# Performance work log

Measured on AMD Instinct MI355X. Metric: run time of the kernel, lower is better.

## Reference

```python
import jax, jax.numpy as jnp
import numpy as np


def setup_inputs() -> dict:
    key = jax.random.key(0)
    k1, k2 = jax.random.split(key)
    N, B, E, H = 2048, 8, 256, 512
    x = jax.random.normal(k1, (N, B, E), dtype=jnp.float32)
    h = jax.random.normal(k2, (N, B, H), dtype=jnp.float32)
    return {"x": x, "h": h}


def reference(x, h):
    # x: (N, B, E), h: (N, B, H)
    H = h.shape[-1]
    xt = jnp.transpose(x, (1, 0, 2))            # (B, N, E)
    norm = jnp.linalg.norm(xt, axis=2, keepdims=True)  # (B, N, 1)
    xn = xt / norm
    # cosine-similarity scores, softmax over keys (last dim)
    scores = jax.nn.softmax(jnp.einsum('bie,bje->bij', xn, xn), axis=2)  # (B, N, N)
    ht = jnp.transpose(h, (1, 0, 2))            # (B, N, H)
    # The original expands scores/h over an H-fold dim, bmm's, and sums;
    # that equals H * (scores @ h). Keep the H factor for faithfulness
    # (it cancels in the global-norm division below).
    g = H * jnp.einsum('bij,bjh->bih', scores, ht)  # (B, N, H)
    g = jnp.transpose(g, (1, 0, 2))             # (N, B, H)
    return g / jnp.linalg.norm(g)
```

## Files before the change

kernel.cpp:

```cpp
#include <hip/hip_runtime.h>
#include <hip/hip_bf16.h>

#define N_TOK 2048
#define B_SZ  8
#define E_DIM 256
#define H_DIM 512
#define ITERS (N_TOK / 32)

typedef __attribute__((ext_vector_type(8))) short bf16x8;
typedef __attribute__((ext_vector_type(4))) float f32x4;

__device__ __forceinline__ unsigned short f2bf(float f) {
    union { float f; unsigned u; } v; v.f = f;
    unsigned r = v.u + 0x7FFF + ((v.u >> 16) & 1);
    return (unsigned short)(r >> 16);
}
__device__ __forceinline__ float bf2f(unsigned short b) {
    union { unsigned u; float f; } v; v.u = ((unsigned)b) << 16;
    return v.f;
}

__global__ void prep_kernel(const float* __restrict__ x,
                            const float* __restrict__ hptr,
                            unsigned short* __restrict__ Xn,
                            unsigned short* __restrict__ Vp) {
    int bid = blockIdx.x;
    int t = threadIdx.x;
    if (bid < N_TOK * B_SZ) {
        int r = bid;
        int i = r >> 3, b = r & 7;
        float v = x[(size_t)r * E_DIM + t];
        float s = v * v;
        #pragma unroll
        for (int o = 32; o > 0; o >>= 1) s += __shfl_xor(s, o);
        __shared__ float red[4];
        int lane = t & 63, w = t >> 6;
        if (lane == 0) red[w] = s;
        __syncthreads();
        float tot = red[0] + red[1] + red[2] + red[3];
        float rn = 1.0f / sqrtf(tot);
        int u = t >> 3, lo = t & 7;
        Xn[((size_t)b * N_TOK + i) * E_DIM + (size_t)((u ^ (i & 7)) * 8 + lo)] =
            f2bf(v * rn);
    } else {
        int lin = bid - N_TOK * B_SZ;
        int jb = lin & 63, hb = (lin >> 6) & 15, b = lin >> 10;
        __shared__ float tile[32][33];
        int j0 = jb * 32, h0 = hb * 32;
        int tx = t & 31, ty = t >> 5;
        #pragma unroll
        for (int it = 0; it < 4; it++) {
            int j = j0 + ty + it * 8;
            tile[ty + it * 8][tx] = hptr[((size_t)j * B_SZ + b) * H_DIM + h0 + tx];
        }
        __syncthreads();
        size_t base = ((size_t)b * (N_TOK / 32) + jb) * (H_DIM * 32);
        #pragma unroll
        for (int it = 0; it < 4; it++) {
            int hc = h0 + ty + it * 8;
            int jg = tx >> 3, swz = (hc >> 1) & 3;
            Vp[base + (size_t)(hc * 4 + (jg ^ swz)) * 8 + (tx & 7)] =
                f2bf(tile[tx][ty + it * 8]);
        }
    }
}

#define PT_STRIDE 40

__launch_bounds__(256, 2)
__global__ void flash_kernel(const unsigned short* __restrict__ Xn,
                             const unsigned short* __restrict__ Vp,
                             float* __restrict__ out,
                             float* __restrict__ sumsq) {
    __shared__ __attribute__((aligned(16))) unsigned short Kbuf[2][32 * 256];
    __shared__ __attribute__((aligned(16))) unsigned short Pt[4][16 * PT_STRIDE];

    int b  = blockIdx.x;
    int q0 = blockIdx.y * 32;
    int t = threadIdx.x;
    int w = t >> 6, lane = t & 63;
    int quad = lane >> 4, nm = lane & 15;
    int rg = w >> 1, hh = w & 1;

    const unsigned short* Kbase = Xn + (size_t)b * N_TOK * E_DIM;
    const unsigned short* Qrow =
        Xn + ((size_t)b * N_TOK + q0 + rg * 16 + nm) * E_DIM;
    const unsigned short* Vtile0 = Vp + (size_t)b * (N_TOK / 32) * (H_DIM * 32);

    bf16x8 qf[8];
    #pragma unroll
    for (int ec = 0; ec < 8; ec++)
        qf[ec] = *(const bf16x8*)(Qrow + (size_t)(((ec * 4 + quad) ^ (nm & 7)) * 8));

    f32x4 O[16];
    #pragma unroll
    for (int i = 0; i < 16; i++) O[i] = (f32x4){0.f, 0.f, 0.f, 0.f};
    float l_lane[4];
    #pragma unroll
    for (int r = 0; r < 4; r++) l_lane[r] = 0.0f;

    auto stage = [&](int tile, int buf) {
        const unsigned short* src0 = Kbase + (size_t)tile * 32 * E_DIM;
        #pragma unroll
        for (int k = 0; k < 4; k++) {
            int chunk = w * 4 + k;
            __builtin_amdgcn_global_load_lds(
                (const __attribute__((address_space(1))) unsigned int*)
                    (src0 + (size_t)chunk * 512 + lane * 8),
                (__attribute__((address_space(3))) unsigned int*)
                    (&Kbuf[buf][chunk * 512]),
                16, 0, 0);
        }
    };

    stage(0, 0);
    int vswz = (quad ^ ((nm >> 1) & 3)) * 8;

    for (int it = 0; it < ITERS; ++it) {
        __syncthreads();
        int cur = it & 1;

        const unsigned short* Vt = Vtile0 + (size_t)it * (H_DIM * 32);
        bf16x8 vf[16];
        #pragma unroll
        for (int tt = 0; tt < 16; tt++) {
            int hc = hh * 256 + tt * 16 + nm;
            vf[tt] = *(const bf16x8*)(Vt + (size_t)(hc * 4) * 8 + vswz);
        }

        if (it + 1 < ITERS) stage(it + 1, cur ^ 1);
        const unsigned short* KB = &Kbuf[cur][0];

        f32x4 s0 = (f32x4){0.f,0.f,0.f,0.f}, s1 = (f32x4){0.f,0.f,0.f,0.f};
        #pragma unroll
        for (int ec = 0; ec < 8; ec++) {
            int u = ((ec * 4 + quad) ^ (nm & 7)) * 8;
            bf16x8 kf0 = *(const bf16x8*)(KB + nm * 256 + u);
            bf16x8 kf1 = *(const bf16x8*)(KB + (16 + nm) * 256 + u);
            s0 = __builtin_amdgcn_mfma_f32_16x16x32_bf16(qf[ec], kf0, s0, 0, 0, 0);
            s1 = __builtin_amdgcn_mfma_f32_16x16x32_bf16(qf[ec], kf1, s1, 0, 0, 0);
        }

        #pragma unroll
        for (int r = 0; r < 4; r++) {
            unsigned short pb0 = f2bf(__expf(s0[r] - 1.0f));
            unsigned short pb1 = f2bf(__expf(s1[r] - 1.0f));
            l_lane[r] += bf2f(pb0) + bf2f(pb1);
            Pt[w][(quad * 4 + r) * PT_STRIDE + nm]      = pb0;
            Pt[w][(quad * 4 + r) * PT_STRIDE + 16 + nm] = pb1;
        }

        asm volatile("s_waitcnt lgkmcnt(0)" ::: "memory");
        __builtin_amdgcn_wave_barrier();
        bf16x8 pf = *(const bf16x8*)(&Pt[w][nm * PT_STRIDE + quad * 8]);

        #pragma unroll
        for (int tt = 0; tt < 16; tt++)
            O[tt] = __builtin_amdgcn_mfma_f32_16x16x32_bf16(pf, vf[tt], O[tt], 0, 0, 0);
    }

    float linv[4];
    #pragma unroll
    for (int r = 0; r < 4; r++) {
        float lv = l_lane[r];
        #pragma unroll
        for (int o = 1; o < 16; o <<= 1) lv += __shfl_xor(lv, o);
        linv[r] = 1.0f / lv;
    }

    float ss = 0.0f;
    #pragma unroll
    for (int tt = 0; tt < 16; tt++) {
        #pragma unroll
        for (int r = 0; r < 4; r++) {
            float val = O[tt][r] * linv[r];
            int row = q0 + rg * 16 + quad * 4 + r;
            int col = hh * 256 + tt * 16 + nm;
            out[((size_t)row * B_SZ + b) * H_DIM + col] = val;
            ss += val * val;
        }
    }
    #pragma unroll
    for (int o = 1; o < 64; o <<= 1) ss += __shfl_xor(ss, o);
    if (lane == 0) atomicAdd(sumsq, ss);
}

__global__ void scale_kernel(float* __restrict__ out,
                             const float* __restrict__ sumsq) {
    size_t idx = ((size_t)blockIdx.x * blockDim.x + threadIdx.x) * 4;
    float rs = 1.0f / sqrtf(*sumsq);
    float4 v = *(float4*)(out + idx);
    v.x *= rs; v.y *= rs; v.z *= rs; v.w *= rs;
    *(float4*)(out + idx) = v;
}

extern "C" void kernel_launch(void* const* d_in, const int* in_sizes, int n_in,
                              void* d_out, int out_size, void* d_ws, size_t ws_size,
                              hipStream_t stream) {
    const float* x = (const float*)d_in[0];
    const float* h = (const float*)d_in[1];
    float* out = (float*)d_out;

    unsigned short* Xn = (unsigned short*)d_ws;
    unsigned short* Vp = Xn + (size_t)B_SZ * N_TOK * E_DIM;
    float* sumsq = (float*)(Vp + (size_t)B_SZ * N_TOK * H_DIM);

    hipMemsetAsync(sumsq, 0, sizeof(float), stream);
    prep_kernel<<<N_TOK * B_SZ + (N_TOK / 32) * (H_DIM / 32) * B_SZ,
                  256, 0, stream>>>(x, h, Xn, Vp);
    flash_kernel<<<dim3(B_SZ, N_TOK / 32), 256, 0, stream>>>(Xn, Vp, out, sumsq);
    scale_kernel<<<out_size / (4 * 256), 256, 0, stream>>>(out, sumsq);
}
```

Measured before the change: 227.1 us.

## Split key range across two wave groups in flash kernel and vectorize prep

The flash kernel now launches 512 threads per block, and two groups of four waves each process half of the key tiles. Their partial O and l accumulators are combined through LDS at the end, before normalization and the sum-of-squares atomic. This roughly doubles the waves in flight per query block, which helps hide latency for a grid of only 512 blocks. It costs more LDS per block, an extra reduction step, and tighter register limits from the 512,4 launch bounds. The prep kernel also switches to one wave per row with float4 loads and packed 4-element bf16 stores for both the X normalization and the V transpose.

```diff
diff --git a/kernel.cpp b/kernel.cpp
--- a/kernel.cpp
+++ b/kernel.cpp
@@ -1,14 +1,14 @@
 #include <hip/hip_runtime.h>
-#include <hip/hip_bf16.h>
 
 #define N_TOK 2048
 #define B_SZ  8
 #define E_DIM 256
 #define H_DIM 512
-#define ITERS (N_TOK / 32)
+#define TPG   (N_TOK / 64)
 
 typedef __attribute__((ext_vector_type(8))) short bf16x8;
 typedef __attribute__((ext_vector_type(4))) float f32x4;
+typedef __attribute__((ext_vector_type(4))) unsigned short u16x4;
 
 __device__ __forceinline__ unsigned short f2bf(float f) {
     union { float f; unsigned u; } v; v.f = f;
@@ -26,24 +26,23 @@
                             unsigned short* __restrict__ Vp) {
     int bid = blockIdx.x;
     int t = threadIdx.x;
-    if (bid < N_TOK * B_SZ) {
-        int r = bid;
-        int i = r >> 3, b = r & 7;
-        float v = x[(size_t)r * E_DIM + t];
-        float s = v * v;
+    if (bid < (N_TOK * B_SZ) / 4) {
+        int w = t >> 6, lane = t & 63;
+        int r = bid * 4 + w;
+        int n = r >> 3, b = r & 7;
+        float4 v = *(const float4*)(x + (size_t)r * E_DIM + lane * 4);
+        float s = v.x * v.x + v.y * v.y + v.z * v.z + v.w * v.w;
         #pragma unroll
         for (int o = 32; o > 0; o >>= 1) s += __shfl_xor(s, o);
-        __shared__ float red[4];
-        int lane = t & 63, w = t >> 6;
-        if (lane == 0) red[w] = s;
-        __syncthreads();
-        float tot = red[0] + red[1] + red[2] + red[3];
-        float rn = 1.0f / sqrtf(tot);
-        int u = t >> 3, lo = t & 7;
-        Xn[((size_t)b * N_TOK + i) * E_DIM + (size_t)((u ^ (i & 7)) * 8 + lo)] =
-            f2bf(v * rn);
+        float rn = 1.0f / sqrtf(s);
+        u16x4 pk;
+        pk[0] = f2bf(v.x * rn); pk[1] = f2bf(v.y * rn);
+        pk[2] = f2bf(v.z * rn); pk[3] = f2bf(v.w * rn);
+        int u = lane >> 1, half = lane & 1;
+        *(u16x4*)(Xn + ((size_t)b * N_TOK + n) * E_DIM
+                     + (size_t)((u ^ (n & 7)) * 8 + half * 4)) = pk;
     } else {
-        int lin = bid - N_TOK * B_SZ;
+        int lin = bid - (N_TOK * B_SZ) / 4;
         int jb = lin & 63, hb = (lin >> 6) & 15, b = lin >> 10;
         __shared__ float tile[32][33];
         int j0 = jb * 32, h0 = hb * 32;
@@ -55,32 +54,33 @@
         }
         __syncthreads();
         size_t base = ((size_t)b * (N_TOK / 32) + jb) * (H_DIM * 32);
-        #pragma unroll
-        for (int it = 0; it < 4; it++) {
-            int hc = h0 + ty + it * 8;
-            int jg = tx >> 3, swz = (hc >> 1) & 3;
-            Vp[base + (size_t)(hc * 4 + (jg ^ swz)) * 8 + (tx & 7)] =
-                f2bf(tile[tx][ty + it * 8]);
-        }
+        int hcl = t >> 3, jg = (t >> 1) & 3, half = t & 1;
+        int hc = h0 + hcl;
+        u16x4 pk;
+        #pragma unroll
+        for (int k = 0; k < 4; k++)
+            pk[k] = f2bf(tile[jg * 8 + half * 4 + k][hcl]);
+        *(u16x4*)(Vp + base + (size_t)(hc * 4 + (jg ^ ((hcl >> 1) & 3))) * 8
+                     + half * 4) = pk;
     }
 }
 
 #define PT_STRIDE 40
 
-__launch_bounds__(256, 2)
+__launch_bounds__(512, 4)
 __global__ void flash_kernel(const unsigned short* __restrict__ Xn,
                              const unsigned short* __restrict__ Vp,
                              float* __restrict__ out,
                              float* __restrict__ sumsq) {
-    __shared__ __attribute__((aligned(16))) unsigned short Kbuf[2][32 * 256];
-    __shared__ __attribute__((aligned(16))) unsigned short Pt[4][16 * PT_STRIDE];
+    __shared__ __attribute__((aligned(16))) unsigned short Kbuf[2][2][32 * 256];
+    __shared__ __attribute__((aligned(16))) unsigned short Pt[8][16 * PT_STRIDE];
 
     int b  = blockIdx.x;
     int q0 = blockIdx.y * 32;
     int t = threadIdx.x;
     int w = t >> 6, lane = t & 63;
     int quad = lane >> 4, nm = lane & 15;
-    int rg = w >> 1, hh = w & 1;
+    int ks = w >> 2, rg = (w >> 1) & 1, hh = w & 1, wl = w & 3;
 
     const unsigned short* Kbase = Xn + (size_t)b * N_TOK * E_DIM;
     const unsigned short* Qrow =
@@ -103,22 +103,24 @@
         const unsigned short* src0 = Kbase + (size_t)tile * 32 * E_DIM;
         #pragma unroll
         for (int k = 0; k < 4; k++) {
-            int chunk = w * 4 + k;
+            int chunk = wl * 4 + k;
             __builtin_amdgcn_global_load_lds(
                 (const __attribute__((address_space(1))) unsigned int*)
                     (src0 + (size_t)chunk * 512 + lane * 8),
                 (__attribute__((address_space(3))) unsigned int*)
-                    (&Kbuf[buf][chunk * 512]),
+                    (&Kbuf[ks][buf][chunk * 512]),
                 16, 0, 0);
         }
     };
 
-    stage(0, 0);
+    int tile0 = ks * TPG;
+    stage(tile0, 0);
     int vswz = (quad ^ ((nm >> 1) & 3)) * 8;
 
-    for (int it = 0; it < ITERS; ++it) {
+    for (int ii = 0; ii < TPG; ++ii) {
         __syncthreads();
-        int cur = it & 1;
+        int cur = ii & 1;
+        int it = tile0 + ii;
 
         const unsigned short* Vt = Vtile0 + (size_t)it * (H_DIM * 32);
         bf16x8 vf[16];
@@ -128,8 +130,8 @@
             vf[tt] = *(const bf16x8*)(Vt + (size_t)(hc * 4) * 8 + vswz);
         }
 
-        if (it + 1 < ITERS) stage(it + 1, cur ^ 1);
-        const unsigned short* KB = &Kbuf[cur][0];
+        if (ii + 1 < TPG) stage(tile0 + ii + 1, cur ^ 1);
+        const unsigned short* KB = &Kbuf[ks][cur][0];
 
         f32x4 s0 = (f32x4){0.f,0.f,0.f,0.f}, s1 = (f32x4){0.f,0.f,0.f,0.f};
         #pragma unroll
@@ -159,30 +161,56 @@
             O[tt] = __builtin_amdgcn_mfma_f32_16x16x32_bf16(pf, vf[tt], O[tt], 0, 0, 0);
     }
 
-    float linv[4];
-    #pragma unroll
-    for (int r = 0; r < 4; r++) {
-        float lv = l_lane[r];
-        #pragma unroll
-        for (int o = 1; o < 16; o <<= 1) lv += __shfl_xor(lv, o);
-        linv[r] = 1.0f / lv;
-    }
-
-    float ss = 0.0f;
-    #pragma unroll
-    for (int tt = 0; tt < 16; tt++) {
+    __syncthreads();
+    float* Ox = (float*)&Kbuf[0][0][0];
+    float* Lx = (float*)&Pt[0][0];
+    int pr = rg * 2 + hh;
+    if (ks == 1) {
+        float* dst = Ox + pr * (16 * 256);
+        #pragma unroll
+        for (int tt = 0; tt < 16; tt++)
+            *(f32x4*)(dst + (tt * 64 + lane) * 4) = O[tt];
+        #pragma unroll
+        for (int r = 0; r < 4; r++)
+            Lx[pr * 256 + lane * 4 + r] = l_lane[r];
+    }
+    __syncthreads();
+    if (ks == 0) {
+        float* src = Ox + pr * (16 * 256);
+        #pragma unroll
+        for (int tt = 0; tt < 16; tt++) {
+            f32x4 o2 = *(const f32x4*)(src + (tt * 64 + lane) * 4);
+            O[tt] += o2;
+        }
+        #pragma unroll
+        for (int r = 0; r < 4; r++)
+            l_lane[r] += Lx[pr * 256 + lane * 4 + r];
+
+        float linv[4];
         #pragma unroll
         for (int r = 0; r < 4; r++) {
-            float val = O[tt][r] * linv[r];
-            int row = q0 + rg * 16 + quad * 4 + r;
-            int col = hh * 256 + tt * 16 + nm;
-            out[((size_t)row * B_SZ + b) * H_DIM + col] = val;
-            ss += val * val;
-        }
-    }
-    #pragma unroll
-    for (int o = 1; o < 64; o <<= 1) ss += __shfl_xor(ss, o);
-    if (lane == 0) atomicAdd(sumsq, ss);
+            float lv = l_lane[r];
+            #pragma unroll
+            for (int o = 1; o < 16; o <<= 1) lv += __shfl_xor(lv, o);
+            linv[r] = 1.0f / lv;
+        }
+
+        float ss = 0.0f;
+        #pragma unroll
+        for (int tt = 0; tt < 16; tt++) {
+            #pragma unroll
+            for (int r = 0; r < 4; r++) {
+                float val = O[tt][r] * linv[r];
+                int row = q0 + rg * 16 + quad * 4 + r;
+                int col = hh * 256 + tt * 16 + nm;
+                out[((size_t)row * B_SZ + b) * H_DIM + col] = val;
+                ss += val * val;
+            }
+        }
+        #pragma unroll
+        for (int o = 1; o < 64; o <<= 1) ss += __shfl_xor(ss, o);
+        if (lane == 0) atomicAdd(sumsq, ss);
+    }
 }
 
 __global__ void scale_kernel(float* __restrict__ out,
@@ -206,8 +234,8 @@
     float* sumsq = (float*)(Vp + (size_t)B_SZ * N_TOK * H_DIM);
 
     hipMemsetAsync(sumsq, 0, sizeof(float), stream);
-    prep_kernel<<<N_TOK * B_SZ + (N_TOK / 32) * (H_DIM / 32) * B_SZ,
+    prep_kernel<<<(N_TOK * B_SZ) / 4 + (N_TOK / 32) * (H_DIM / 32) * B_SZ,
                   256, 0, stream>>>(x, h, Xn, Vp);
-    flash_kernel<<<dim3(B_SZ, N_TOK / 32), 256, 0, stream>>>(Xn, Vp, out, sumsq);
+    flash_kernel<<<dim3(B_SZ, N_TOK / 32), 512, 0, stream>>>(Xn, Vp, out, sumsq);
     scale_kernel<<<out_size / (4 * 256), 256, 0, stream>>>(out, sumsq);
 }
```

After: 759.1 us. 3.34x slower.
